# Kernel tuning notes

Hardware: AMD Instinct MI355X
Metric: run time of the kernel (lower is better)

Reference implementation:

```python
import jax, jax.numpy as jnp
import numpy as np

D_MODEL = 2048
N_HEAD = 16
B, T = 2, 2048
D_HEAD = D_MODEL // N_HEAD          # 128
D_Q = D_MODEL // 3                  # 682
D_KV = D_MODEL // 2                 # 1024
D_QK_N = D_HEAD // 2                # 64
D_QK_R = D_HEAD // 2                # 64
LN_EPS = 1e-5


def setup_inputs() -> dict:
    key = jax.random.key(0)
    ks = jax.random.split(key, 8)
    s = 0.02
    return {
        'x': jax.random.normal(ks[0], (B, T, D_MODEL), dtype=jnp.float32),
        'Wdq_w': jax.random.normal(ks[1], (D_Q, D_MODEL), dtype=jnp.float32) * s,
        'Wdq_b': jnp.zeros((D_Q,), jnp.float32),
        'qn_g': jnp.ones((D_Q,), jnp.float32),
        'qn_b': jnp.zeros((D_Q,), jnp.float32),
        'Wuq_w': jax.random.normal(ks[2], (D_MODEL, D_Q), dtype=jnp.float32) * s,
        'Wuq_b': jnp.zeros((D_MODEL,), jnp.float32),
        'Wdkv_w': jax.random.normal(ks[3], (D_KV + D_QK_R, D_MODEL), dtype=jnp.float32) * s,
        'Wdkv_b': jnp.zeros((D_KV + D_QK_R,), jnp.float32),
        'kvn_g': jnp.ones((D_KV,), jnp.float32),
        'kvn_b': jnp.zeros((D_KV,), jnp.float32),
        'Wukv_w': jax.random.normal(ks[4], (D_MODEL + N_HEAD * D_QK_N, D_KV), dtype=jnp.float32) * s,
        'Wukv_b': jnp.zeros((D_MODEL + N_HEAD * D_QK_N,), jnp.float32),
        'Wo_w': jax.random.normal(ks[5], (D_MODEL, D_MODEL), dtype=jnp.float32) * s,
        'Wo_b': jnp.zeros((D_MODEL,), jnp.float32),
    }


def _linear(x, w, b):
    return jnp.einsum('...i,oi->...o', x, w) + b


def _layernorm(x, g, b):
    mu = jnp.mean(x, axis=-1, keepdims=True)
    var = jnp.mean(jnp.square(x - mu), axis=-1, keepdims=True)
    return (x - mu) * jax.lax.rsqrt(var + LN_EPS) * g + b


def _rotary(x):
    # Faithful to source: positions are taken from axis 1 of x (B, A, T, d)
    A, d = x.shape[1], x.shape[-1]
    inv_freq = (1.0 / 10000.0) ** (jnp.arange(0, d, 2, dtype=jnp.float32) / d)
    freqs = jnp.arange(A, dtype=jnp.float32)[:, None] * inv_freq[None, :]
    cos = jnp.cos(freqs)[None, :, None, :]
    sin = jnp.sin(freqs)[None, :, None, :]
    x1, x2 = jnp.split(x, 2, axis=-1)
    return jnp.concatenate([x1 * cos + x2 * sin, -x1 * sin + x2 * cos], axis=-1)


def reference(x, Wdq_w, Wdq_b, qn_g, qn_b, Wuq_w, Wuq_b,
              Wdkv_w, Wdkv_b, kvn_g, kvn_b, Wukv_w, Wukv_b, Wo_w, Wo_b):
    Bx, Tx, C = x.shape
    # Q path: down-proj -> norm -> up-proj
    c_q = _layernorm(_linear(x, Wdq_w, Wdq_b), qn_g, qn_b)
    q = _linear(c_q, Wuq_w, Wuq_b).reshape(Bx, Tx, N_HEAD, D_HEAD).transpose(0, 2, 1, 3)
    q_n, q_r = q[..., :D_QK_N], q[..., D_QK_N:]
    q_r = _rotary(q_r)
    # KV path
    c_kv = _linear(x, Wdkv_w, Wdkv_b)
    kv_n, k_r = c_kv[..., :D_KV], c_kv[..., D_KV:]
    kv_n = _layernorm(kv_n, kvn_g, kvn_b)
    kv = _linear(kv_n, Wukv_w, Wukv_b).reshape(Bx, Tx, N_HEAD, D_HEAD + D_QK_N).transpose(0, 2, 1, 3)
    k_n, v = kv[..., :D_QK_N], kv[..., D_QK_N:]
    k_r = k_r.reshape(Bx, Tx, 1, D_QK_R).transpose(0, 2, 1, 3)  # (B,1,T,dr)
    k_r = _rotary(k_r)  # identity here (single position), kept for fidelity
    k_r = jnp.broadcast_to(k_r, (Bx, N_HEAD, Tx, D_QK_R))
    q_full = jnp.concatenate([q_n, q_r], axis=-1)   # (B,H,T,d_head)
    k_full = jnp.concatenate([k_n, k_r], axis=-1)   # (B,H,T,d_head)
    # causal SDPA (scale = 1/sqrt(q dim))
    scale = 1.0 / np.sqrt(D_HEAD)
    scores = jnp.einsum('bhqd,bhkd->bhqk', q_full, k_full) * scale
    causal = jnp.tril(jnp.ones((Tx, Tx), dtype=bool))
    scores = jnp.where(causal[None, None], scores, jnp.finfo(scores.dtype).min)
    p = jax.nn.softmax(scores, axis=-1)
    y = jnp.einsum('bhqk,bhkd->bhqd', p, v)
    y = y.transpose(0, 2, 1, 3).reshape(Bx, Tx, C)
    return _linear(y, Wo_w, Wo_b)
```

## Files before the change

kernel.cpp:

```cpp
#include <hip/hip_runtime.h>
#include <math.h>

#define TOK 4096
#define DM 2048
#define DQ 682
#define DQP 704
#define DKV 1024
#define DUKV 3072
#define NH 16
#define T_SEQ 2048
#define NQKV 1792

typedef __attribute__((ext_vector_type(8))) short short8;
typedef __attribute__((ext_vector_type(4))) float floatx4;
typedef __attribute__((ext_vector_type(2))) unsigned int uint2v;

__device__ __forceinline__ unsigned short f2bf(float f) {
  union { float f; unsigned int u; } v; v.f = f;
  unsigned int u = v.u;
  u += 0x7fffu + ((u >> 16) & 1u);
  return (unsigned short)(u >> 16);
}
__device__ __forceinline__ unsigned short f2bf_fast(float f) {
  union { float f; unsigned int u; } v; v.f = f;
  return (unsigned short)((v.u + 0x8000u) >> 16);
}

typedef __attribute__((address_space(1))) const unsigned int as1_u32;
typedef __attribute__((address_space(3))) unsigned int as3_u32;
__device__ __forceinline__ void async16(const void* g, void* l) {
  __builtin_amdgcn_global_load_lds((as1_u32*)g, (as3_u32*)l, 16, 0, 0);
}

__global__ __launch_bounds__(256) void gemm_bf16_db(
    const unsigned short* __restrict__ A, int lda,
    const unsigned short* __restrict__ B, int ldb,
    const float* __restrict__ bias, float* __restrict__ C, int ldc,
    int Nvalid, int K)
{
  __shared__ __align__(16) unsigned short sm[16384];
  const int tid = threadIdx.x;
  const int w = tid >> 6;
  const int lane = tid & 63;
  const int q = lane >> 4;
  const int r = lane & 15;
  const int bm = blockIdx.y * 128;
  const int bn = blockIdx.x * 128;

  floatx4 acc[4][4];
#pragma unroll
  for (int i = 0; i < 4; i++)
#pragma unroll
    for (int j = 0; j < 4; j++) acc[i][j] = (floatx4){0.f, 0.f, 0.f, 0.f};

  const int srow = tid >> 2;
  const int scol = (tid & 3) * 8;
  const unsigned short* Ag0 = A + (size_t)(bm + srow) * lda + scol;
  const unsigned short* Ag1 = A + (size_t)(bm + 64 + srow) * lda + scol;
  const unsigned short* Bg0 = B + (size_t)(bn + srow) * ldb + scol;
  const unsigned short* Bg1 = B + (size_t)(bn + 64 + srow) * ldb + scol;

  const int mrow0 = (w >> 1) * 64;
  const int ncol0 = (w & 1) * 64;

  async16(Ag0, &sm[w * 512]);
  async16(Ag1, &sm[2048 + w * 512]);
  async16(Bg0, &sm[8192 + w * 512]);
  async16(Bg1, &sm[8192 + 2048 + w * 512]);

  for (int k0 = 0; k0 < K; k0 += 32) {
    const int cur = (k0 >> 5) & 1;
    __syncthreads();
    if (k0 + 32 < K) {
      const int nxt = cur ^ 1;
      async16(Ag0 + k0 + 32, &sm[nxt * 4096 + w * 512]);
      async16(Ag1 + k0 + 32, &sm[nxt * 4096 + 2048 + w * 512]);
      async16(Bg0 + k0 + 32, &sm[8192 + nxt * 4096 + w * 512]);
      async16(Bg1 + k0 + 32, &sm[8192 + nxt * 4096 + 2048 + w * 512]);
    }
    const unsigned short* As = &sm[cur * 4096];
    const unsigned short* Bs = &sm[8192 + cur * 4096];
    short8 a[4], b[4];
#pragma unroll
    for (int i = 0; i < 4; i++)
      a[i] = *(const short8*)&As[(mrow0 + i * 16 + r) * 32 + q * 8];
#pragma unroll
    for (int j = 0; j < 4; j++)
      b[j] = *(const short8*)&Bs[(ncol0 + j * 16 + r) * 32 + q * 8];
#pragma unroll
    for (int i = 0; i < 4; i++)
#pragma unroll
      for (int j = 0; j < 4; j++)
        acc[i][j] = __builtin_amdgcn_mfma_f32_16x16x32_bf16(a[i], b[j], acc[i][j], 0, 0, 0);
  }

#pragma unroll
  for (int j = 0; j < 4; j++) {
    int gc = bn + ncol0 + j * 16 + r;
    if (gc >= Nvalid) continue;
    float bv = bias[gc];
#pragma unroll
    for (int i = 0; i < 4; i++) {
#pragma unroll
      for (int v = 0; v < 4; v++) {
        int gr = bm + mrow0 + i * 16 + q * 4 + v;
        C[(size_t)gr * ldc + gc] = acc[i][j][v] + bv;
      }
    }
  }
}

__global__ __launch_bounds__(256) void gemm_dqkv(
    const unsigned short* __restrict__ A,
    const unsigned short* __restrict__ B,
    const float* __restrict__ bias, float* __restrict__ C,
    unsigned short* __restrict__ Kr)
{
  __shared__ __align__(16) unsigned short sm[16384];
  const int tid = threadIdx.x;
  const int w = tid >> 6;
  const int lane = tid & 63;
  const int q = lane >> 4;
  const int r = lane & 15;
  const int bm = blockIdx.y * 128;
  const int bn = blockIdx.x * 128;
  const int K = 2048;

  floatx4 acc[4][4];
#pragma unroll
  for (int i = 0; i < 4; i++)
#pragma unroll
    for (int j = 0; j < 4; j++) acc[i][j] = (floatx4){0.f, 0.f, 0.f, 0.f};

  const int srow = tid >> 2;
  const int scol = (tid & 3) * 8;
  const unsigned short* Ag0 = A + (size_t)(bm + srow) * K + scol;
  const unsigned short* Ag1 = A + (size_t)(bm + 64 + srow) * K + scol;
  const unsigned short* Bg0 = B + (size_t)(bn + srow) * K + scol;
  const unsigned short* Bg1 = B + (size_t)(bn + 64 + srow) * K + scol;

  const int mrow0 = (w >> 1) * 64;
  const int ncol0 = (w & 1) * 64;

  async16(Ag0, &sm[w * 512]);
  async16(Ag1, &sm[2048 + w * 512]);
  async16(Bg0, &sm[8192 + w * 512]);
  async16(Bg1, &sm[8192 + 2048 + w * 512]);

  for (int k0 = 0; k0 < K; k0 += 32) {
    const int cur = (k0 >> 5) & 1;
    __syncthreads();
    if (k0 + 32 < K) {
      const int nxt = cur ^ 1;
      async16(Ag0 + k0 + 32, &sm[nxt * 4096 + w * 512]);
      async16(Ag1 + k0 + 32, &sm[nxt * 4096 + 2048 + w * 512]);
      async16(Bg0 + k0 + 32, &sm[8192 + nxt * 4096 + w * 512]);
      async16(Bg1 + k0 + 32, &sm[8192 + nxt * 4096 + 2048 + w * 512]);
    }
    const unsigned short* As = &sm[cur * 4096];
    const unsigned short* Bs = &sm[8192 + cur * 4096];
    short8 a[4], b[4];
#pragma unroll
    for (int i = 0; i < 4; i++)
      a[i] = *(const short8*)&As[(mrow0 + i * 16 + r) * 32 + q * 8];
#pragma unroll
    for (int j = 0; j < 4; j++)
      b[j] = *(const short8*)&Bs[(ncol0 + j * 16 + r) * 32 + q * 8];
#pragma unroll
    for (int i = 0; i < 4; i++)
#pragma unroll
      for (int j = 0; j < 4; j++)
        acc[i][j] = __builtin_amdgcn_mfma_f32_16x16x32_bf16(a[i], b[j], acc[i][j], 0, 0, 0);
  }

#pragma unroll
  for (int j = 0; j < 4; j++) {
    int gc = bn + ncol0 + j * 16 + r;
    float bv = bias[gc];
    const bool rope = (gc >= 1728);
    const int dr = gc - 1728;
#pragma unroll
    for (int i = 0; i < 4; i++) {
#pragma unroll
      for (int v = 0; v < 4; v++) {
        int gr = bm + mrow0 + i * 16 + q * 4 + v;
        float val = acc[i][j][v] + bv;
        C[(size_t)gr * NQKV + gc] = val;
        if (rope) {
          int bb = gr >> 11, tt = gr & 2047;
          Kr[((size_t)(bb * 32 + (tt >> 6))) * 4096 + (dr >> 5) * 2048 +
             (tt & 63) * 32 + (dr & 31)] = f2bf(val);
        }
      }
    }
  }
}

__global__ __launch_bounds__(256) void gemm_up_fused(
    const unsigned short* __restrict__ Aq, const unsigned short* __restrict__ Bq,
    const float* __restrict__ biasq, unsigned short* __restrict__ Qall,
    const unsigned short* __restrict__ Akv, const unsigned short* __restrict__ Bkv,
    const float* __restrict__ biaskv,
    unsigned short* __restrict__ Kn, unsigned short* __restrict__ Vb)
{
  __shared__ __align__(16) unsigned short sm[16384];
  const int tid = threadIdx.x;
  const int w = tid >> 6;
  const int lane = tid & 63;
  const int q = lane >> 4;
  const int r = lane & 15;
  const int bx = blockIdx.x;
  const bool isQ = bx < 16;
  const int bn = isQ ? bx * 128 : (bx - 16) * 128;
  const int bm = blockIdx.y * 128;
  const int K = isQ ? DQP : DKV;
  const unsigned short* A = isQ ? Aq : Akv;
  const unsigned short* B = isQ ? Bq : Bkv;

  floatx4 acc[4][4];
#pragma unroll
  for (int i = 0; i < 4; i++)
#pragma unroll
    for (int j = 0; j < 4; j++) acc[i][j] = (floatx4){0.f, 0.f, 0.f, 0.f};

  const int srow = tid >> 2;
  const int scol = (tid & 3) * 8;
  const unsigned short* Ag0 = A + (size_t)(bm + srow) * K + scol;
  const unsigned short* Ag1 = A + (size_t)(bm + 64 + srow) * K + scol;
  const unsigned short* Bg0 = B + (size_t)(bn + srow) * K + scol;
  const unsigned short* Bg1 = B + (size_t)(bn + 64 + srow) * K + scol;

  const int mrow0 = (w >> 1) * 64;
  const int ncol0 = (w & 1) * 64;

  async16(Ag0, &sm[w * 512]);
  async16(Ag1, &sm[2048 + w * 512]);
  async16(Bg0, &sm[8192 + w * 512]);
  async16(Bg1, &sm[8192 + 2048 + w * 512]);

  for (int k0 = 0; k0 < K; k0 += 32) {
    const int cur = (k0 >> 5) & 1;
    __syncthreads();
    if (k0 + 32 < K) {
      const int nxt = cur ^ 1;
      async16(Ag0 + k0 + 32, &sm[nxt * 4096 + w * 512]);
      async16(Ag1 + k0 + 32, &sm[nxt * 4096 + 2048 + w * 512]);
      async16(Bg0 + k0 + 32, &sm[8192 + nxt * 4096 + w * 512]);
      async16(Bg1 + k0 + 32, &sm[8192 + nxt * 4096 + 2048 + w * 512]);
    }
    const unsigned short* As = &sm[cur * 4096];
    const unsigned short* Bs = &sm[8192 + cur * 4096];
    short8 a[4], b[4];
#pragma unroll
    for (int i = 0; i < 4; i++)
      a[i] = *(const short8*)&As[(mrow0 + i * 16 + r) * 32 + q * 8];
#pragma unroll
    for (int j = 0; j < 4; j++)
      b[j] = *(const short8*)&Bs[(ncol0 + j * 16 + r) * 32 + q * 8];
#pragma unroll
    for (int i = 0; i < 4; i++)
#pragma unroll
      for (int j = 0; j < 4; j++)
        acc[i][j] = __builtin_amdgcn_mfma_f32_16x16x32_bf16(a[i], b[j], acc[i][j], 0, 0, 0);
  }

  if (!isQ) {
#pragma unroll
    for (int j = 0; j < 4; j++) {
      int gc = bn + ncol0 + j * 16 + r;
      float bv = biaskv[gc];
      int hh = gc / 192;
      int rel = gc - hh * 192;
#pragma unroll
      for (int i = 0; i < 4; i++) {
#pragma unroll
        for (int v = 0; v < 4; v++) {
          int gr = bm + mrow0 + i * 16 + q * 4 + v;
          int bb = gr >> 11, tt = gr & 2047;
          int bhh = bb * NH + hh;
          int kt = tt >> 6;
          unsigned short val = f2bf(acc[i][j][v] + bv);
          if (rel < 64) {
            Kn[((size_t)(bhh * 32 + kt)) * 4096 + (rel >> 5) * 2048 +
               (tt & 63) * 32 + (rel & 31)] = val;
          } else {
            int d = rel - 64;
            Vb[((size_t)(bhh * 32 + kt)) * 8192 + ((tt >> 5) & 1) * 4096 +
               d * 32 + (tt & 31)] = val;
          }
        }
      }
    }
    return;
  }

  const int h = bx;
  const float QS = (float)(0.08838834764831845 * 1.4426950408889634);
  if ((w & 1) == 0) {
#pragma unroll
    for (int j = 0; j < 4; j++) {
      int d = j * 16 + r;
      float bv = biasq[h * 128 + d];
#pragma unroll
      for (int i = 0; i < 4; i++) {
#pragma unroll
        for (int v = 0; v < 4; v++) {
          int gr = bm + mrow0 + i * 16 + q * 4 + v;
          int bb = gr >> 11, t = gr & 2047;
          Qall[(((size_t)(bb * NH + h)) * T_SEQ + t) * 128 + d] =
              f2bf((acc[i][j][v] + bv) * QS);
        }
      }
    }
  } else {
    float cs[2], sn[2], bv1[2], bv2[2];
#pragma unroll
    for (int jp = 0; jp < 2; jp++) {
      int jj = jp * 16 + r;
      float ang = (float)h * exp2f(-(float)jj * (13.287712379549449f / 32.0f));
      cs[jp] = cosf(ang); sn[jp] = sinf(ang);
      bv1[jp] = biasq[h * 128 + 64 + jj];
      bv2[jp] = biasq[h * 128 + 96 + jj];
    }
#pragma unroll
    for (int i = 0; i < 4; i++) {
#pragma unroll
      for (int v = 0; v < 4; v++) {
        int gr = bm + mrow0 + i * 16 + q * 4 + v;
        int bb = gr >> 11, t = gr & 2047;
        unsigned short* Qr = Qall + (((size_t)(bb * NH + h)) * T_SEQ + t) * 128;
#pragma unroll
        for (int jp = 0; jp < 2; jp++) {
          int jj = jp * 16 + r;
          float x1 = acc[i][jp][v] + bv1[jp];
          float x2 = acc[i][jp + 2][v] + bv2[jp];
          Qr[64 + jj] = f2bf((x1 * cs[jp] + x2 * sn[jp]) * QS);
          Qr[96 + jj] = f2bf((x2 * cs[jp] - x1 * sn[jp]) * QS);
        }
      }
    }
  }
}

__global__ __launch_bounds__(256) void cvt_bf16_pad(
    const float* __restrict__ in, unsigned short* __restrict__ out,
    int irows, int icols, int ocols, long total)
{
  long idx = (long)blockIdx.x * 256 + threadIdx.x;
  if (idx >= total) return;
  int rr = (int)(idx / ocols);
  int cc = (int)(idx - (long)rr * ocols);
  out[idx] = (rr < irows && cc < icols) ? f2bf(in[(size_t)rr * icols + cc]) : 0;
}

__device__ __forceinline__ void cvt_region(
    const float* __restrict__ in, unsigned short* __restrict__ out,
    int irows, int icols, int ocols, long idx)
{
  int rr = (int)(idx / ocols);
  int cc = (int)(idx - (long)rr * ocols);
  out[idx] = (rr < irows && cc < icols) ? f2bf(in[(size_t)rr * icols + cc]) : 0;
}

__global__ __launch_bounds__(256) void prep_weights(
    const float* __restrict__ Wdq_w, const float* __restrict__ Wdkv_w,
    const float* __restrict__ Wuq_w, const float* __restrict__ Wukv_w,
    const float* __restrict__ Wo_w,
    const float* __restrict__ Wdq_b, const float* __restrict__ Wdkv_b,
    unsigned short* __restrict__ Wqkv_bf, unsigned short* __restrict__ Wuq_bf,
    unsigned short* __restrict__ Wukv_bf, unsigned short* __restrict__ Wo_bf,
    float* __restrict__ bias_qkv)
{
  const long bx = blockIdx.x;
  if (bx < 5632) {
    cvt_region(Wdq_w, Wqkv_bf, 682, 2048, 2048, bx * 256 + threadIdx.x);
  } else if (bx < 14336) {
    cvt_region(Wdkv_w, Wqkv_bf + 704L * 2048, 1088, 2048, 2048,
               (bx - 5632) * 256 + threadIdx.x);
  } else if (bx < 19968) {
    cvt_region(Wuq_w, Wuq_bf, 2048, 682, 704, (bx - 14336) * 256 + threadIdx.x);
  } else if (bx < 32256) {
    cvt_region(Wukv_w, Wukv_bf, 3072, 1024, 1024, (bx - 19968) * 256 + threadIdx.x);
  } else if (bx < 48640) {
    cvt_region(Wo_w, Wo_bf, 2048, 2048, 2048, (bx - 32256) * 256 + threadIdx.x);
  } else {
    int i = (int)(bx - 48640) * 256 + threadIdx.x;
    if (i < NQKV)
      bias_qkv[i] = (i < DQ) ? Wdq_b[i] : ((i < DQP) ? 0.f : Wdkv_b[i - DQP]);
  }
}

__device__ __forceinline__ float block_sum(float v, float* sbuf) {
#pragma unroll
  for (int off = 32; off > 0; off >>= 1) v += __shfl_down(v, off, 64);
  int wid = threadIdx.x >> 6;
  __syncthreads();
  if ((threadIdx.x & 63) == 0) sbuf[wid] = v;
  __syncthreads();
  return sbuf[0] + sbuf[1] + sbuf[2] + sbuf[3];
}

__global__ __launch_bounds__(256) void ln_dual(
    const float* __restrict__ cqkv,
    unsigned short* __restrict__ outq, unsigned short* __restrict__ outkv,
    const float* __restrict__ qg, const float* __restrict__ qb,
    const float* __restrict__ kg, const float* __restrict__ kb)
{
  __shared__ float sbuf[4];
  const int row = blockIdx.x;
  const bool isQ = row < 4096;
  const int r2 = isQ ? row : row - 4096;
  const float* xr = cqkv + (size_t)r2 * NQKV + (isQ ? 0 : DQP);
  const int D = isQ ? DQ : DKV;
  const int ocols = isQ ? DQP : DKV;
  const float* g = isQ ? qg : kg;
  const float* bta = isQ ? qb : kb;
  unsigned short* orow = (isQ ? outq : outkv) + (size_t)r2 * ocols;

  float s = 0.f;
  for (int i = threadIdx.x; i < D; i += 256) s += xr[i];
  float mu = block_sum(s, sbuf) / (float)D;
  float v = 0.f;
  for (int i = threadIdx.x; i < D; i += 256) { float d = xr[i] - mu; v += d * d; }
  float var = block_sum(v, sbuf) / (float)D;
  float rstd = rsqrtf(var + 1e-5f);
  for (int i = threadIdx.x; i < ocols; i += 256)
    orow[i] = (i < D) ? f2bf((xr[i] - mu) * rstd * g[i] + bta[i]) : 0;
}

__global__ __launch_bounds__(256, 2) void attn_mfma4(
    const unsigned short* __restrict__ Qall,
    const unsigned short* __restrict__ Kn,
    const unsigned short* __restrict__ Kr,
    const unsigned short* __restrict__ Vb,
    unsigned short* __restrict__ y)
{
  __shared__ __align__(16) unsigned short sm[37376];
  const int id = (int)blockIdx.x;
  const int bhid = id & 31;
  const int xx = id >> 5;
  const int qt = (xx < 8) ? xx : (23 - xx);
  const int h = bhid & 15, b = bhid >> 4;
  const int tid = threadIdx.x;
  const int w = tid >> 6, lane = tid & 63, q = lane >> 4, r = lane & 15;
  const int bh = bhid;

  short8 qb[2][4];
#pragma unroll
  for (int g = 0; g < 2; g++) {
    const unsigned short* Qrow =
        Qall + ((size_t)bh * T_SEQ + (size_t)qt * 128 + w * 32 + g * 16 + r) * 128 + q * 8;
#pragma unroll
    for (int c = 0; c < 4; c++) qb[g][c] = *(const short8*)(Qrow + c * 32);
  }

  floatx4 oacc[2][8];
#pragma unroll
  for (int g = 0; g < 2; g++)
#pragma unroll
    for (int jd = 0; jd < 8; jd++) oacc[g][jd] = (floatx4){0.f, 0.f, 0.f, 0.f};
  float m_i[2] = {-3.0e38f, -3.0e38f}, l_i[2] = {0.f, 0.f};

  const char* KnG = (const char*)(Kn + (size_t)bh * 32 * 4096);
  const char* KrG = (const char*)(Kr + (size_t)b * 32 * 4096);
  const char* VG  = (const char*)(Vb + (size_t)bh * 32 * 8192);
  char* smB = (char*)sm;
  unsigned short* Psw = sm + 32768 + w * 1152;
  const int ktmax = 2 * qt + 1;

#pragma unroll
  for (int i = 0; i < 2; i++) {
    async16(KnG + i * 4096 + w * 1024 + lane * 16, smB + i * 4096 + w * 1024);
    async16(KrG + i * 4096 + w * 1024 + lane * 16, smB + 8192 + i * 4096 + w * 1024);
  }
#pragma unroll
  for (int i = 0; i < 4; i++)
    async16(VG + i * 4096 + w * 1024 + lane * 16, smB + 32768 + i * 4096 + w * 1024);

  for (int kt = 0; kt <= ktmax; kt++) {
    const int cur = kt & 1;
    __syncthreads();
    if (kt < ktmax) {
      const int nxt = cur ^ 1;
      const char* kn = KnG + (size_t)(kt + 1) * 8192;
      const char* kr = KrG + (size_t)(kt + 1) * 8192;
      const char* vg = VG + (size_t)(kt + 1) * 16384;
      char* kd = smB + nxt * 16384;
      char* vd = smB + 32768 + nxt * 16384;
#pragma unroll
      for (int i = 0; i < 2; i++) {
        async16(kn + i * 4096 + w * 1024 + lane * 16, kd + i * 4096 + w * 1024);
        async16(kr + i * 4096 + w * 1024 + lane * 16, kd + 8192 + i * 4096 + w * 1024);
      }
#pragma unroll
      for (int i = 0; i < 4; i++)
        async16(vg + i * 4096 + w * 1024 + lane * 16, vd + i * 4096 + w * 1024);
    }

    const bool activeW = (kt * 64 <= qt * 128 + w * 32 + 31);
    if (activeW) {
      const unsigned short* KsC = sm + cur * 8192;
      const unsigned short* VsC = sm + 16384 + cur * 8192;

      floatx4 sacc[2][4];
#pragma unroll
      for (int g = 0; g < 2; g++)
#pragma unroll
        for (int j = 0; j < 4; j++) sacc[g][j] = (floatx4){0.f, 0.f, 0.f, 0.f};
#pragma unroll
      for (int c = 0; c < 4; c++) {
        short8 ak[4];
#pragma unroll
        for (int j = 0; j < 4; j++)
          ak[j] = *(const short8*)&KsC[c * 2048 + (j * 16 + r) * 32 + q * 8];
#pragma unroll
        for (int g = 0; g < 2; g++)
#pragma unroll
          for (int j = 0; j < 4; j++)
            sacc[g][j] = __builtin_amdgcn_mfma_f32_16x16x32_bf16(ak[j], qb[g][c], sacc[g][j], 0, 0, 0);
      }

#pragma unroll
      for (int g = 0; g < 2; g++) {
        float sv[16];
#pragma unroll
        for (int j = 0; j < 4; j++)
#pragma unroll
          for (int v = 0; v < 4; v++) sv[j * 4 + v] = sacc[g][j][v];
        const int rel = qt * 128 + w * 32 + g * 16 + r - kt * 64;
        if (rel < 63) {
#pragma unroll
          for (int j = 0; j < 4; j++)
#pragma unroll
            for (int v = 0; v < 4; v++)
              if (j * 16 + q * 4 + v > rel) sv[j * 4 + v] = -3.0e38f;
        }
        float rm = sv[0];
#pragma unroll
        for (int t16 = 1; t16 < 16; t16++) rm = fmaxf(rm, sv[t16]);
        rm = fmaxf(rm, __shfl_xor(rm, 16, 64));
        rm = fmaxf(rm, __shfl_xor(rm, 32, 64));
        float mnew = fmaxf(m_i[g], rm);
        float alpha = exp2f(m_i[g] - mnew);
        m_i[g] = mnew;
        float p[16], rsum = 0.f;
#pragma unroll
        for (int t16 = 0; t16 < 16; t16++) { p[t16] = exp2f(sv[t16] - mnew); rsum += p[t16]; }
        rsum += __shfl_xor(rsum, 16, 64);
        rsum += __shfl_xor(rsum, 32, 64);
        l_i[g] = l_i[g] * alpha + rsum;
#pragma unroll
        for (int jd = 0; jd < 8; jd++) {
          oacc[g][jd][0] *= alpha; oacc[g][jd][1] *= alpha;
          oacc[g][jd][2] *= alpha; oacc[g][jd][3] *= alpha;
        }
#pragma unroll
        for (int j = 0; j < 4; j++) {
          unsigned int lo = (unsigned int)f2bf_fast(p[j * 4 + 0]) |
                            ((unsigned int)f2bf_fast(p[j * 4 + 1]) << 16);
          unsigned int hi = (unsigned int)f2bf_fast(p[j * 4 + 2]) |
                            ((unsigned int)f2bf_fast(p[j * 4 + 3]) << 16);
          uint2v pk; pk[0] = lo; pk[1] = hi;
          *(uint2v*)&Psw[r * 72 + j * 16 + q * 4] = pk;
        }
#pragma unroll
        for (int c2 = 0; c2 < 2; c2++) {
          short8 pb = *(const short8*)&Psw[r * 72 + c2 * 32 + q * 8];
#pragma unroll
          for (int jd = 0; jd < 8; jd++) {
            short8 bv = *(const short8*)&VsC[c2 * 4096 + (jd * 16 + r) * 32 + q * 8];
            oacc[g][jd] = __builtin_amdgcn_mfma_f32_16x16x32_bf16(bv, pb, oacc[g][jd], 0, 0, 0);
          }
        }
      }
    }
  }

#pragma unroll
  for (int g = 0; g < 2; g++) {
    float inv = 1.0f / l_i[g];
    unsigned short* yr =
        y + ((size_t)(b * T_SEQ) + (size_t)qt * 128 + w * 32 + g * 16 + r) * DM + h * 128;
#pragma unroll
    for (int jd = 0; jd < 8; jd++) {
      unsigned short o0 = f2bf(oacc[g][jd][0] * inv);
      unsigned short o1 = f2bf(oacc[g][jd][1] * inv);
      unsigned short o2 = f2bf(oacc[g][jd][2] * inv);
      unsigned short o3 = f2bf(oacc[g][jd][3] * inv);
      unsigned int lo = (unsigned int)o0 | ((unsigned int)o1 << 16);
      unsigned int hi = (unsigned int)o2 | ((unsigned int)o3 << 16);
      unsigned int* dst = (unsigned int*)(yr + jd * 16 + q * 4);
      dst[0] = lo; dst[1] = hi;
    }
  }
}

extern "C" void kernel_launch(void* const* d_in, const int* in_sizes, int n_in,
                              void* d_out, int out_size, void* d_ws, size_t ws_size,
                              hipStream_t stream) {
  const float* x      = (const float*)d_in[0];
  const float* Wdq_w  = (const float*)d_in[1];
  const float* Wdq_b  = (const float*)d_in[2];
  const float* qn_g   = (const float*)d_in[3];
  const float* qn_b   = (const float*)d_in[4];
  const float* Wuq_w  = (const float*)d_in[5];
  const float* Wuq_b  = (const float*)d_in[6];
  const float* Wdkv_w = (const float*)d_in[7];
  const float* Wdkv_b = (const float*)d_in[8];
  const float* kvn_g  = (const float*)d_in[9];
  const float* kvn_b  = (const float*)d_in[10];
  const float* Wukv_w = (const float*)d_in[11];
  const float* Wukv_b = (const float*)d_in[12];
  const float* Wo_w   = (const float*)d_in[13];
  const float* Wo_b   = (const float*)d_in[14];
  float* out = (float*)d_out;

  float* ws = (float*)d_ws;
  unsigned short* x_bf    = (unsigned short*)(ws);
  unsigned short* y_bf    = (unsigned short*)(ws);
  unsigned short* Wqkv_bf = (unsigned short*)(ws + 4194304);
  unsigned short* Wuq_bf  = (unsigned short*)(ws + 6029312);
  unsigned short* Wukv_bf = (unsigned short*)(ws + 6750208);
  float* bias_qkv = ws + 8323072;
  float* c_qkv    = ws + 8324864;
  unsigned short* c_q_bf = (unsigned short*)(ws + 15664896);
  unsigned short* kvn_bf = (unsigned short*)(ws + 17106688);
  unsigned short* Q_all  = (unsigned short*)(ws + 19203840);
  unsigned short* Kn_blk = (unsigned short*)(ws + 23398144);
  unsigned short* Kr_blk = (unsigned short*)(ws + 25495296);
  unsigned short* V_blk  = (unsigned short*)(ws + 25626368);
  unsigned short* Wo_bf  = (unsigned short*)(ws + 29820672);

  dim3 blk(256);

  cvt_bf16_pad<<<(4096L*2048 + 255) / 256, blk, 0, stream>>>(x, x_bf, 4096, 2048, 2048, 4096L*2048);
  prep_weights<<<48647, blk, 0, stream>>>(Wdq_w, Wdkv_w, Wuq_w, Wukv_w, Wo_w,
                                          Wdq_b, Wdkv_b,
                                          Wqkv_bf, Wuq_bf, Wukv_bf, Wo_bf, bias_qkv);

  gemm_dqkv<<<dim3(14, 32), blk, 0, stream>>>(x_bf, Wqkv_bf, bias_qkv, c_qkv, Kr_blk);
  ln_dual<<<8192, blk, 0, stream>>>(c_qkv, c_q_bf, kvn_bf, qn_g, qn_b, kvn_g, kvn_b);
  gemm_up_fused<<<dim3(40, 32), blk, 0, stream>>>(c_q_bf, Wuq_bf, Wuq_b, Q_all,
                                                  kvn_bf, Wukv_bf, Wukv_b,
                                                  Kn_blk, V_blk);
  attn_mfma4<<<512, blk, 0, stream>>>(Q_all, Kn_blk, Kr_blk, V_blk, y_bf);
  gemm_bf16_db<<<dim3(16, 32), blk, 0, stream>>>(y_bf, 2048, Wo_bf, 2048, Wo_b, out, DM, DM, 2048);
}
```

Baseline: 429.4 us.

## Split-K the down-projection GEMM, fuse reduction into LayerNorm, merge prep kernels

```diff
diff --git a/kernel.cpp b/kernel.cpp
--- a/kernel.cpp
+++ b/kernel.cpp
@@ -32,20 +32,21 @@
   __builtin_amdgcn_global_load_lds((as1_u32*)g, (as3_u32*)l, 16, 0, 0);
 }
 
-__global__ __launch_bounds__(256) void gemm_bf16_db(
-    const unsigned short* __restrict__ A, int lda,
-    const unsigned short* __restrict__ B, int ldb,
-    const float* __restrict__ bias, float* __restrict__ C, int ldc,
-    int Nvalid, int K)
+__global__ __launch_bounds__(256) void gemm_dqkv_sk(
+    const unsigned short* __restrict__ A,
+    const unsigned short* __restrict__ B,
+    float* __restrict__ P0, float* __restrict__ P1)
 {
   __shared__ __align__(16) unsigned short sm[16384];
+  const int kz = blockIdx.z;
+  const unsigned short* Ab = A + kz * 1024;
+  const unsigned short* Bb = B + kz * 1024;
+  float* C = kz ? P1 : P0;
+  const int K = 1024;
+
   const int tid = threadIdx.x;
-  const int w = tid >> 6;
-  const int lane = tid & 63;
-  const int q = lane >> 4;
-  const int r = lane & 15;
-  const int bm = blockIdx.y * 128;
-  const int bn = blockIdx.x * 128;
+  const int w = tid >> 6, lane = tid & 63, q = lane >> 4, r = lane & 15;
+  const int bm = blockIdx.y * 128, bn = blockIdx.x * 128;
 
   floatx4 acc[4][4];
 #pragma unroll
@@ -53,15 +54,12 @@
 #pragma unroll
     for (int j = 0; j < 4; j++) acc[i][j] = (floatx4){0.f, 0.f, 0.f, 0.f};
 
-  const int srow = tid >> 2;
-  const int scol = (tid & 3) * 8;
-  const unsigned short* Ag0 = A + (size_t)(bm + srow) * lda + scol;
-  const unsigned short* Ag1 = A + (size_t)(bm + 64 + srow) * lda + scol;
-  const unsigned short* Bg0 = B + (size_t)(bn + srow) * ldb + scol;
-  const unsigned short* Bg1 = B + (size_t)(bn + 64 + srow) * ldb + scol;
-
-  const int mrow0 = (w >> 1) * 64;
-  const int ncol0 = (w & 1) * 64;
+  const int srow = tid >> 2, scol = (tid & 3) * 8;
+  const unsigned short* Ag0 = Ab + (size_t)(bm + srow) * 2048 + scol;
+  const unsigned short* Ag1 = Ab + (size_t)(bm + 64 + srow) * 2048 + scol;
+  const unsigned short* Bg0 = Bb + (size_t)(bn + srow) * 2048 + scol;
+  const unsigned short* Bg1 = Bb + (size_t)(bn + 64 + srow) * 2048 + scol;
+  const int mrow0 = (w >> 1) * 64, ncol0 = (w & 1) * 64;
 
   async16(Ag0, &sm[w * 512]);
   async16(Ag1, &sm[2048 + w * 512]);
@@ -97,34 +95,26 @@
 #pragma unroll
   for (int j = 0; j < 4; j++) {
     int gc = bn + ncol0 + j * 16 + r;
-    if (gc >= Nvalid) continue;
-    float bv = bias[gc];
 #pragma unroll
     for (int i = 0; i < 4; i++) {
 #pragma unroll
       for (int v = 0; v < 4; v++) {
         int gr = bm + mrow0 + i * 16 + q * 4 + v;
-        C[(size_t)gr * ldc + gc] = acc[i][j][v] + bv;
-      }
-    }
-  }
-}
-
-__global__ __launch_bounds__(256) void gemm_dqkv(
+        C[(size_t)gr * NQKV + gc] = acc[i][j][v];
+      }
+    }
+  }
+}
+
+__global__ __launch_bounds__(256) void gemm_wo64(
     const unsigned short* __restrict__ A,
     const unsigned short* __restrict__ B,
-    const float* __restrict__ bias, float* __restrict__ C,
-    unsigned short* __restrict__ Kr)
+    const float* __restrict__ bias, float* __restrict__ C)
 {
-  __shared__ __align__(16) unsigned short sm[16384];
+  __shared__ __align__(16) unsigned short sm[32768];
   const int tid = threadIdx.x;
-  const int w = tid >> 6;
-  const int lane = tid & 63;
-  const int q = lane >> 4;
-  const int r = lane & 15;
-  const int bm = blockIdx.y * 128;
-  const int bn = blockIdx.x * 128;
-  const int K = 2048;
+  const int w = tid >> 6, lane = tid & 63, q = lane >> 4, r = lane & 15;
+  const int bm = blockIdx.y * 128, bn = blockIdx.x * 128;
 
   floatx4 acc[4][4];
 #pragma unroll
@@ -132,65 +122,63 @@
 #pragma unroll
     for (int j = 0; j < 4; j++) acc[i][j] = (floatx4){0.f, 0.f, 0.f, 0.f};
 
-  const int srow = tid >> 2;
-  const int scol = (tid & 3) * 8;
-  const unsigned short* Ag0 = A + (size_t)(bm + srow) * K + scol;
-  const unsigned short* Ag1 = A + (size_t)(bm + 64 + srow) * K + scol;
-  const unsigned short* Bg0 = B + (size_t)(bn + srow) * K + scol;
-  const unsigned short* Bg1 = B + (size_t)(bn + 64 + srow) * K + scol;
-
-  const int mrow0 = (w >> 1) * 64;
-  const int ncol0 = (w & 1) * 64;
-
-  async16(Ag0, &sm[w * 512]);
-  async16(Ag1, &sm[2048 + w * 512]);
-  async16(Bg0, &sm[8192 + w * 512]);
-  async16(Bg1, &sm[8192 + 2048 + w * 512]);
-
-  for (int k0 = 0; k0 < K; k0 += 32) {
-    const int cur = (k0 >> 5) & 1;
+  const int srow = tid >> 2, scol = (tid & 3) * 8;
+  const unsigned short* Ag0 = A + (size_t)(bm + srow) * 2048 + scol;
+  const unsigned short* Ag1 = A + (size_t)(bm + 64 + srow) * 2048 + scol;
+  const unsigned short* Bg0 = B + (size_t)(bn + srow) * 2048 + scol;
+  const unsigned short* Bg1 = B + (size_t)(bn + 64 + srow) * 2048 + scol;
+  const int mrow0 = (w >> 1) * 64, ncol0 = (w & 1) * 64;
+
+#pragma unroll
+  for (int c2 = 0; c2 < 2; c2++) {
+    async16(Ag0 + c2 * 32, &sm[c2 * 4096 + w * 512]);
+    async16(Ag1 + c2 * 32, &sm[c2 * 4096 + 2048 + w * 512]);
+    async16(Bg0 + c2 * 32, &sm[16384 + c2 * 4096 + w * 512]);
+    async16(Bg1 + c2 * 32, &sm[16384 + c2 * 4096 + 2048 + w * 512]);
+  }
+
+  for (int k0 = 0; k0 < 2048; k0 += 64) {
+    const int cur = (k0 >> 6) & 1;
     __syncthreads();
-    if (k0 + 32 < K) {
+    if (k0 + 64 < 2048) {
       const int nxt = cur ^ 1;
-      async16(Ag0 + k0 + 32, &sm[nxt * 4096 + w * 512]);
-      async16(Ag1 + k0 + 32, &sm[nxt * 4096 + 2048 + w * 512]);
-      async16(Bg0 + k0 + 32, &sm[8192 + nxt * 4096 + w * 512]);
-      async16(Bg1 + k0 + 32, &sm[8192 + nxt * 4096 + 2048 + w * 512]);
-    }
-    const unsigned short* As = &sm[cur * 4096];
-    const unsigned short* Bs = &sm[8192 + cur * 4096];
-    short8 a[4], b[4];
-#pragma unroll
-    for (int i = 0; i < 4; i++)
-      a[i] = *(const short8*)&As[(mrow0 + i * 16 + r) * 32 + q * 8];
-#pragma unroll
-    for (int j = 0; j < 4; j++)
-      b[j] = *(const short8*)&Bs[(ncol0 + j * 16 + r) * 32 + q * 8];
-#pragma unroll
-    for (int i = 0; i < 4; i++)
+#pragma unroll
+      for (int c2 = 0; c2 < 2; c2++) {
+        async16(Ag0 + k0 + 64 + c2 * 32, &sm[nxt * 8192 + c2 * 4096 + w * 512]);
+        async16(Ag1 + k0 + 64 + c2 * 32, &sm[nxt * 8192 + c2 * 4096 + 2048 + w * 512]);
+        async16(Bg0 + k0 + 64 + c2 * 32, &sm[16384 + nxt * 8192 + c2 * 4096 + w * 512]);
+        async16(Bg1 + k0 + 64 + c2 * 32, &sm[16384 + nxt * 8192 + c2 * 4096 + 2048 + w * 512]);
+      }
+    }
+#pragma unroll
+    for (int c2 = 0; c2 < 2; c2++) {
+      const unsigned short* As = &sm[cur * 8192 + c2 * 4096];
+      const unsigned short* Bs = &sm[16384 + cur * 8192 + c2 * 4096];
+      short8 a[4], b[4];
+#pragma unroll
+      for (int i = 0; i < 4; i++)
+        a[i] = *(const short8*)&As[(mrow0 + i * 16 + r) * 32 + q * 8];
 #pragma unroll
       for (int j = 0; j < 4; j++)
-        acc[i][j] = __builtin_amdgcn_mfma_f32_16x16x32_bf16(a[i], b[j], acc[i][j], 0, 0, 0);
+        b[j] = *(const short8*)&Bs[(ncol0 + j * 16 + r) * 32 + q * 8];
+#pragma unroll
+      for (int i = 0; i < 4; i++)
+#pragma unroll
+        for (int j = 0; j < 4; j++)
+          acc[i][j] = __builtin_amdgcn_mfma_f32_16x16x32_bf16(a[i], b[j], acc[i][j], 0, 0, 0);
+    }
   }
 
 #pragma unroll
   for (int j = 0; j < 4; j++) {
     int gc = bn + ncol0 + j * 16 + r;
     float bv = bias[gc];
-    const bool rope = (gc >= 1728);
-    const int dr = gc - 1728;
 #pragma unroll
     for (int i = 0; i < 4; i++) {
 #pragma unroll
       for (int v = 0; v < 4; v++) {
         int gr = bm + mrow0 + i * 16 + q * 4 + v;
-        float val = acc[i][j][v] + bv;
-        C[(size_t)gr * NQKV + gc] = val;
-        if (rope) {
-          int bb = gr >> 11, tt = gr & 2047;
-          Kr[((size_t)(bb * 32 + (tt >> 6))) * 4096 + (dr >> 5) * 2048 +
-             (tt & 63) * 32 + (dr & 31)] = f2bf(val);
-        }
+        C[(size_t)gr * 2048 + gc] = acc[i][j][v] + bv;
       }
     }
   }
@@ -205,10 +193,7 @@
 {
   __shared__ __align__(16) unsigned short sm[16384];
   const int tid = threadIdx.x;
-  const int w = tid >> 6;
-  const int lane = tid & 63;
-  const int q = lane >> 4;
-  const int r = lane & 15;
+  const int w = tid >> 6, lane = tid & 63, q = lane >> 4, r = lane & 15;
   const int bx = blockIdx.x;
   const bool isQ = bx < 16;
   const int bn = isQ ? bx * 128 : (bx - 16) * 128;
@@ -223,15 +208,12 @@
 #pragma unroll
     for (int j = 0; j < 4; j++) acc[i][j] = (floatx4){0.f, 0.f, 0.f, 0.f};
 
-  const int srow = tid >> 2;
-  const int scol = (tid & 3) * 8;
+  const int srow = tid >> 2, scol = (tid & 3) * 8;
   const unsigned short* Ag0 = A + (size_t)(bm + srow) * K + scol;
   const unsigned short* Ag1 = A + (size_t)(bm + 64 + srow) * K + scol;
   const unsigned short* Bg0 = B + (size_t)(bn + srow) * K + scol;
   const unsigned short* Bg1 = B + (size_t)(bn + 64 + srow) * K + scol;
-
-  const int mrow0 = (w >> 1) * 64;
-  const int ncol0 = (w & 1) * 64;
+  const int mrow0 = (w >> 1) * 64, ncol0 = (w & 1) * 64;
 
   async16(Ag0, &sm[w * 512]);
   async16(Ag1, &sm[2048 + w * 512]);
@@ -342,17 +324,6 @@
   }
 }
 
-__global__ __launch_bounds__(256) void cvt_bf16_pad(
-    const float* __restrict__ in, unsigned short* __restrict__ out,
-    int irows, int icols, int ocols, long total)
-{
-  long idx = (long)blockIdx.x * 256 + threadIdx.x;
-  if (idx >= total) return;
-  int rr = (int)(idx / ocols);
-  int cc = (int)(idx - (long)rr * ocols);
-  out[idx] = (rr < irows && cc < icols) ? f2bf(in[(size_t)rr * icols + cc]) : 0;
-}
-
 __device__ __forceinline__ void cvt_region(
     const float* __restrict__ in, unsigned short* __restrict__ out,
     int irows, int icols, int ocols, long idx)
@@ -362,70 +333,97 @@
   out[idx] = (rr < irows && cc < icols) ? f2bf(in[(size_t)rr * icols + cc]) : 0;
 }
 
-__global__ __launch_bounds__(256) void prep_weights(
+__global__ __launch_bounds__(256) void prep_all(
+    const float* __restrict__ x,
     const float* __restrict__ Wdq_w, const float* __restrict__ Wdkv_w,
     const float* __restrict__ Wuq_w, const float* __restrict__ Wukv_w,
     const float* __restrict__ Wo_w,
     const float* __restrict__ Wdq_b, const float* __restrict__ Wdkv_b,
+    unsigned short* __restrict__ x_bf,
     unsigned short* __restrict__ Wqkv_bf, unsigned short* __restrict__ Wuq_bf,
     unsigned short* __restrict__ Wukv_bf, unsigned short* __restrict__ Wo_bf,
     float* __restrict__ bias_qkv)
 {
   const long bx = blockIdx.x;
-  if (bx < 5632) {
-    cvt_region(Wdq_w, Wqkv_bf, 682, 2048, 2048, bx * 256 + threadIdx.x);
-  } else if (bx < 14336) {
+  if (bx < 32768) {
+    long idx = bx * 256 + threadIdx.x;
+    x_bf[idx] = f2bf(x[idx]);
+  } else if (bx < 38400) {
+    cvt_region(Wdq_w, Wqkv_bf, 682, 2048, 2048, (bx - 32768) * 256 + threadIdx.x);
+  } else if (bx < 47104) {
     cvt_region(Wdkv_w, Wqkv_bf + 704L * 2048, 1088, 2048, 2048,
-               (bx - 5632) * 256 + threadIdx.x);
-  } else if (bx < 19968) {
-    cvt_region(Wuq_w, Wuq_bf, 2048, 682, 704, (bx - 14336) * 256 + threadIdx.x);
-  } else if (bx < 32256) {
-    cvt_region(Wukv_w, Wukv_bf, 3072, 1024, 1024, (bx - 19968) * 256 + threadIdx.x);
-  } else if (bx < 48640) {
-    cvt_region(Wo_w, Wo_bf, 2048, 2048, 2048, (bx - 32256) * 256 + threadIdx.x);
+               (bx - 38400) * 256 + threadIdx.x);
+  } else if (bx < 52736) {
+    cvt_region(Wuq_w, Wuq_bf, 2048, 682, 704, (bx - 47104) * 256 + threadIdx.x);
+  } else if (bx < 65024) {
+    cvt_region(Wukv_w, Wukv_bf, 3072, 1024, 1024, (bx - 52736) * 256 + threadIdx.x);
+  } else if (bx < 81408) {
+    cvt_region(Wo_w, Wo_bf, 2048, 2048, 2048, (bx - 65024) * 256 + threadIdx.x);
   } else {
-    int i = (int)(bx - 48640) * 256 + threadIdx.x;
+    int i = (int)(bx - 81408) * 256 + threadIdx.x;
     if (i < NQKV)
       bias_qkv[i] = (i < DQ) ? Wdq_b[i] : ((i < DQP) ? 0.f : Wdkv_b[i - DQP]);
   }
 }
 
-__device__ __forceinline__ float block_sum(float v, float* sbuf) {
-#pragma unroll
-  for (int off = 32; off > 0; off >>= 1) v += __shfl_down(v, off, 64);
-  int wid = threadIdx.x >> 6;
-  __syncthreads();
-  if ((threadIdx.x & 63) == 0) sbuf[wid] = v;
-  __syncthreads();
-  return sbuf[0] + sbuf[1] + sbuf[2] + sbuf[3];
-}
-
-__global__ __launch_bounds__(256) void ln_dual(
-    const float* __restrict__ cqkv,
+__global__ __launch_bounds__(256) void ln_dual_r(
+    const float* __restrict__ p0, const float* __restrict__ p1,
+    const float* __restrict__ bqkv,
     unsigned short* __restrict__ outq, unsigned short* __restrict__ outkv,
-    const float* __restrict__ qg, const float* __restrict__ qb,
-    const float* __restrict__ kg, const float* __restrict__ kb)
+    unsigned short* __restrict__ Kr,
+    const float* __restrict__ qg, const float* __restrict__ qb2,
+    const float* __restrict__ kg, const float* __restrict__ kb2)
 {
-  __shared__ float sbuf[4];
-  const int row = blockIdx.x;
-  const bool isQ = row < 4096;
-  const int r2 = isQ ? row : row - 4096;
-  const float* xr = cqkv + (size_t)r2 * NQKV + (isQ ? 0 : DQP);
+  __shared__ float sbuf[8];
+  const int blk = blockIdx.x;
+  if (blk >= 8192) {
+    const int base = (blk - 8192) * 512;
+#pragma unroll
+    for (int s = 0; s < 2; s++) {
+      int idx = base + s * 256 + threadIdx.x;
+      int row = idx >> 6, dr = idx & 63;
+      size_t off = (size_t)row * NQKV + 1728 + dr;
+      float v = p0[off] + p1[off] + bqkv[1728 + dr];
+      Kr[((size_t)((row >> 11) * 32 + ((row & 2047) >> 6))) * 4096 +
+         (dr >> 5) * 2048 + (row & 63) * 32 + (dr & 31)] = f2bf(v);
+    }
+    return;
+  }
+  const bool isQ = blk < 4096;
+  const int r2 = isQ ? blk : blk - 4096;
+  const int off = isQ ? 0 : DQP;
+  const float* x0 = p0 + (size_t)r2 * NQKV + off;
+  const float* x1 = p1 + (size_t)r2 * NQKV + off;
+  const float* bb = bqkv + off;
   const int D = isQ ? DQ : DKV;
   const int ocols = isQ ? DQP : DKV;
   const float* g = isQ ? qg : kg;
-  const float* bta = isQ ? qb : kb;
+  const float* bta = isQ ? qb2 : kb2;
   unsigned short* orow = (isQ ? outq : outkv) + (size_t)r2 * ocols;
 
-  float s = 0.f;
-  for (int i = threadIdx.x; i < D; i += 256) s += xr[i];
-  float mu = block_sum(s, sbuf) / (float)D;
-  float v = 0.f;
-  for (int i = threadIdx.x; i < D; i += 256) { float d = xr[i] - mu; v += d * d; }
-  float var = block_sum(v, sbuf) / (float)D;
+  float s = 0.f, s2 = 0.f;
+  for (int i = threadIdx.x; i < D; i += 256) {
+    float v = x0[i] + x1[i] + bb[i];
+    s += v; s2 += v * v;
+  }
+#pragma unroll
+  for (int o = 32; o > 0; o >>= 1) {
+    s += __shfl_down(s, o, 64);
+    s2 += __shfl_down(s2, o, 64);
+  }
+  int wid = threadIdx.x >> 6;
+  __syncthreads();
+  if ((threadIdx.x & 63) == 0) { sbuf[wid] = s; sbuf[4 + wid] = s2; }
+  __syncthreads();
+  float su = sbuf[0] + sbuf[1] + sbuf[2] + sbuf[3];
+  float sq = sbuf[4] + sbuf[5] + sbuf[6] + sbuf[7];
+  float mu = su / (float)D;
+  float var = sq / (float)D - mu * mu;
   float rstd = rsqrtf(var + 1e-5f);
-  for (int i = threadIdx.x; i < ocols; i += 256)
-    orow[i] = (i < D) ? f2bf((xr[i] - mu) * rstd * g[i] + bta[i]) : 0;
+  for (int i = threadIdx.x; i < ocols; i += 256) {
+    float v = (i < D) ? ((x0[i] + x1[i] + bb[i]) - mu) * rstd * g[i] + bta[i] : 0.f;
+    orow[i] = (i < D) ? f2bf(v) : 0;
+  }
 }
 
 __global__ __launch_bounds__(256, 2) void attn_mfma4(
@@ -622,27 +620,28 @@
   unsigned short* Wuq_bf  = (unsigned short*)(ws + 6029312);
   unsigned short* Wukv_bf = (unsigned short*)(ws + 6750208);
   float* bias_qkv = ws + 8323072;
-  float* c_qkv    = ws + 8324864;
-  unsigned short* c_q_bf = (unsigned short*)(ws + 15664896);
-  unsigned short* kvn_bf = (unsigned short*)(ws + 17106688);
-  unsigned short* Q_all  = (unsigned short*)(ws + 19203840);
-  unsigned short* Kn_blk = (unsigned short*)(ws + 23398144);
-  unsigned short* Kr_blk = (unsigned short*)(ws + 25495296);
-  unsigned short* V_blk  = (unsigned short*)(ws + 25626368);
-  unsigned short* Wo_bf  = (unsigned short*)(ws + 29820672);
+  float* p0       = ws + 8324864;
+  float* p1       = ws + 15664896;
+  unsigned short* c_q_bf = (unsigned short*)(ws + 23004928);
+  unsigned short* kvn_bf = (unsigned short*)(ws + 24446720);
+  unsigned short* Q_all  = (unsigned short*)(ws + 26543872);
+  unsigned short* Kn_blk = (unsigned short*)(ws + 30738176);
+  unsigned short* Kr_blk = (unsigned short*)(ws + 32835328);
+  unsigned short* V_blk  = (unsigned short*)(ws + 32966400);
+  unsigned short* Wo_bf  = (unsigned short*)(ws + 37160704);
 
   dim3 blk(256);
 
-  cvt_bf16_pad<<<(4096L*2048 + 255) / 256, blk, 0, stream>>>(x, x_bf, 4096, 2048, 2048, 4096L*2048);
-  prep_weights<<<48647, blk, 0, stream>>>(Wdq_w, Wdkv_w, Wuq_w, Wukv_w, Wo_w,
-                                          Wdq_b, Wdkv_b,
-                                          Wqkv_bf, Wuq_bf, Wukv_bf, Wo_bf, bias_qkv);
-
-  gemm_dqkv<<<dim3(14, 32), blk, 0, stream>>>(x_bf, Wqkv_bf, bias_qkv, c_qkv, Kr_blk);
-  ln_dual<<<8192, blk, 0, stream>>>(c_qkv, c_q_bf, kvn_bf, qn_g, qn_b, kvn_g, kvn_b);
+  prep_all<<<81415, blk, 0, stream>>>(x, Wdq_w, Wdkv_w, Wuq_w, Wukv_w, Wo_w,
+                                      Wdq_b, Wdkv_b,
+                                      x_bf, Wqkv_bf, Wuq_bf, Wukv_bf, Wo_bf,
+                                      bias_qkv);
+  gemm_dqkv_sk<<<dim3(14, 32, 2), blk, 0, stream>>>(x_bf, Wqkv_bf, p0, p1);
+  ln_dual_r<<<8704, blk, 0, stream>>>(p0, p1, bias_qkv, c_q_bf, kvn_bf, Kr_blk,
+                                      qn_g, qn_b, kvn_g, kvn_b);
   gemm_up_fused<<<dim3(40, 32), blk, 0, stream>>>(c_q_bf, Wuq_bf, Wuq_b, Q_all,
                                                   kvn_bf, Wukv_bf, Wukv_b,
                                                   Kn_blk, V_blk);
   attn_mfma4<<<512, blk, 0, stream>>>(Q_all, Kn_blk, Kr_blk, V_blk, y_bf);
-  gemm_bf16_db<<<dim3(16, 32), blk, 0, stream>>>(y_bf, 2048, Wo_bf, 2048, Wo_b, out, DM, DM, 2048);
-}
+  gemm_wo64<<<dim3(16, 32), blk, 0, stream>>>(y_bf, Wo_bf, Wo_b, out);
+}
```

New measurement: 419.2 us. 1.02x faster.
